# Performance work log

Measured on AMD Instinct MI355X. Metric: run time of the kernel, lower is better.

## Reference

```python
import jax, jax.numpy as jnp
import numpy as np

H, W = 512, 1024            # panorama resolution
GRID = 512                  # occupancy histogram resolution (height=width=512)
ABS_SCALE = 20000.0         # mm, ground-plane extent
UNIT_SCALE = 1000.0         # m -> mm
COUNT_TH = 100.0            # histogram count clamp


def _xyz_sphere(ref_plan):
    # Vectorized version of the original double loop.
    i = np.arange(H, dtype=np.float32)
    j = np.arange(W, dtype=np.float32)
    theta = -np.pi * (i / (H - 1) - 0.5)          # [H]
    phi = np.pi * (2.0 * j / (W - 1) - 1.0)       # [W]
    ct, st = np.cos(theta)[:, None], np.sin(theta)[:, None]   # [H,1]
    cp, sp = np.cos(phi)[None, :], np.sin(phi)[None, :]       # [1,W]
    if ref_plan == 'horizontal':
        P = np.stack([cp * ct, sp * ct, np.broadcast_to(st, (H, W))], 0)
    elif ref_plan == 'vertical':
        P = np.stack([cp * ct, np.broadcast_to(-st, (H, W)), sp * ct], 0)
    else:  # lateral
        P = np.stack([sp * ct, np.broadcast_to(-st, (H, W)), cp * ct], 0)
    return jnp.asarray(P.astype(np.float32))      # [3,H,W]

_SPHERES = [_xyz_sphere(p) for p in ('horizontal', 'vertical', 'lateral')]


def _density_one(depth_hw, sph):
    # depth_hw: [H,W]; sph: [3,H,W]
    ps = depth_hw[None] * sph                               # [3,H,W] 3D points
    xy = ps[:2].reshape(2, -1) * UNIT_SCALE                 # [2,N] mm, (x,y)
    coords = (xy + ABS_SCALE / 2.0) / ABS_SCALE * GRID      # [2,N] in grid units
    coords = jnp.clip(jnp.round(coords), 0.0, GRID - 1).astype(jnp.int32)
    flat = coords[1] * GRID + coords[0]                     # density[y, x]
    hist = jnp.zeros(GRID * GRID, jnp.float32).at[flat].add(1.0)
    hist = jnp.minimum(hist, COUNT_TH)
    hist = hist / jnp.max(hist)
    return hist.reshape(GRID, GRID)


def _density(depth, sph):
    # depth: [B,1,H,W] -> [B,GRID,GRID], batched scatter histogram
    return jax.vmap(_density_one, in_axes=(0, None))(depth[:, 0], sph)


def _inverse_huber(pred, gt):
    # berHu loss: L1 below c = 0.2*max|d|, scaled L2 above.
    diff = jnp.abs(pred - gt)
    c = 0.2 * jnp.max(diff)
    loss = jnp.where(diff <= c, diff, (diff * diff + c * c) / (2.0 * c))
    return jnp.mean(loss)


def setup_inputs() -> dict:
    key = jax.random.key(0)
    k1, k2 = jax.random.split(key)
    # indoor depths in [0, 10) meters so histogram bins are populated
    pred = jax.random.uniform(k1, (16, 1, H, W), jnp.float32) * 10.0
    gt = jax.random.uniform(k2, (16, 1, H, W), jnp.float32) * 10.0
    return {"pred_depth": pred, "gt_depth": gt}


def reference(pred_depth, gt_depth):
    total = jnp.float32(0.0)
    for sph in _SPHERES:  # fixed 3 projection planes
        pred_om = _density(pred_depth, sph)
        gt_om = _density(gt_depth, sph)
        total = total + _inverse_huber(pred_om, gt_om)
    return total
```

## Files before the change

kernel.cpp:

```cpp
#include <hip/hip_runtime.h>

#define PI_F 3.14159265358979323846f

#define MAXZ_OFF_B   24576
#define HIST_OFF_B   32768
#define BUCK_OFF_B   25198592
#define REGION_U16   12320

__device__ inline float div20000(float a) {
    const float r = 1.0f / 20000.0f;
    float q0 = a * r;
    float e = fmaf(-20000.0f, q0, a);
    return fmaf(e, r, q0);
}

__device__ inline int bin1(float v) {
    float f = rintf(div20000(v + 10000.0f) * 512.0f);
    return (int)fminf(fmaxf(f, 0.0f), 511.0f);
}

__global__ __launch_bounds__(256) void trig_kernel(
    float* __restrict__ tbl, unsigned* __restrict__ maxz,
    float* __restrict__ out) {
    const int t = threadIdx.x + blockIdx.x * 256;
    if (blockIdx.x == 0) {
        if (threadIdx.x < 128) maxz[threadIdx.x] = 0u;
        if (threadIdx.x == 128) out[0] = 0.0f;
    }
    if (t < 1024) {
        float fj = (float)t;
        float phi = PI_F * ((2.0f * fj) / 1023.0f - 1.0f);
        tbl[t] = cosf(phi);
        tbl[1024 + t] = sinf(phi);
    } else {
        int i = t - 1024;
        float fi = (float)i;
        float theta = -PI_F * (fi / 511.0f - 0.5f);
        tbl[2048 + i] = cosf(theta);
        tbl[2560 + i] = sinf(theta);
    }
}

__global__ __launch_bounds__(256) void bin_kernel(
    const float* __restrict__ pred, const float* __restrict__ gt,
    const float* __restrict__ tbl, unsigned short* __restrict__ buck) {
    __shared__ unsigned cnt[768];
    __shared__ unsigned bsum[24];
    __shared__ unsigned off[25];
    __shared__ __align__(16) unsigned short sdata[12288];
    const int tid = threadIdx.x, wg = blockIdx.x;
    const unsigned rep = (unsigned)(tid & 31);
    const int xcd = wg & 7, i4 = (wg >> 3) & 127, hh = wg >> 10;
    const int h = (hh << 3) | xcd;
    #pragma unroll
    for (int z = 0; z < 3; ++z) cnt[tid + (z << 8)] = 0u;
    const float4 cp4 = *(const float4*)&tbl[tid << 2];
    const float4 sp4 = *(const float4*)&tbl[1024 + (tid << 2)];
    const float4 ct4 = *(const float4*)&tbl[2048 + (i4 << 2)];
    const float4 st4 = *(const float4*)&tbl[2560 + (i4 << 2)];
    __syncthreads();
    const float* img = ((h >> 4) ? gt : pred) + ((h & 15) << 19);
    unsigned items[48];
    #pragma unroll
    for (int r = 0; r < 4; ++r) {
        const int i = i4 * 4 + r;
        const float4 d4 = *(const float4*)(img + (i << 10) + (tid << 2));
        const float ct = (&ct4.x)[r], st = (&st4.x)[r];
        #pragma unroll
        for (int k = 0; k < 4; ++k) {
            float d = (&d4.x)[k];
            float aA = (&cp4.x)[k] * ct;
            float aB = (&sp4.x)[k] * ct;
            float A = (d * aA) * 1000.0f;
            float B = (d * aB) * 1000.0f;
            float C = (d * (-st)) * 1000.0f;
            int iA = bin1(A), iB = bin1(B), iC = bin1(C);
            unsigned f0 = ((unsigned)iB << 9) | (unsigned)iA;
            unsigned f1 = ((unsigned)iC << 9) | (unsigned)iA;
            unsigned f2 = ((unsigned)iC << 9) | (unsigned)iB;
            unsigned b0 = f0 >> 15;
            unsigned b1 = 8u + (f1 >> 15);
            unsigned b2 = 16u + (f2 >> 15);
            unsigned r0 = atomicAdd(&cnt[(b0 << 5) | rep], 1u);
            unsigned r1 = atomicAdd(&cnt[(b1 << 5) | rep], 1u);
            unsigned r2 = atomicAdd(&cnt[(b2 << 5) | rep], 1u);
            const int base = (r * 4 + k) * 3;
            items[base + 0] = (b0 << 27) | (rep << 22) | (r0 << 15) | (f0 & 32767u);
            items[base + 1] = (b1 << 27) | (rep << 22) | (r1 << 15) | (f1 & 32767u);
            items[base + 2] = (b2 << 27) | (rep << 22) | (r2 << 15) | (f2 & 32767u);
        }
    }
    __syncthreads();
    if (tid < 24) {
        unsigned s = 0;
        #pragma unroll
        for (int r = 0; r < 32; ++r) {
            unsigned t = cnt[(tid << 5) | r];
            cnt[(tid << 5) | r] = s;
            s += t;
        }
        bsum[tid] = s;
    }
    __syncthreads();
    if (tid == 0) {
        unsigned s = 0;
        #pragma unroll
        for (int b = 0; b < 24; ++b) { off[b] = s; s += bsum[b]; }
        off[24] = s;
    }
    __syncthreads();
    if (tid < 24) {
        unsigned o = off[tid];
        #pragma unroll
        for (int r = 0; r < 32; ++r) cnt[(tid << 5) | r] += o;
    }
    __syncthreads();
    #pragma unroll
    for (int t = 0; t < 48; ++t) {
        const unsigned it = items[t];
        const unsigned slot = ((it >> 27) << 5) | ((it >> 22) & 31u);
        sdata[cnt[slot] + ((it >> 15) & 127u)] = (unsigned short)(it & 32767u);
    }
    __syncthreads();
    unsigned short* regG = buck + (size_t)wg * REGION_U16;
    if (tid < 25) regG[tid] = (unsigned short)off[tid];
    const uint4* s4p = (const uint4*)sdata;
    uint4* g4 = (uint4*)(regG + 32);
    #pragma unroll
    for (int c = 0; c < 6; ++c) g4[(c << 8) + tid] = s4p[(c << 8) + tid];
}

__global__ __launch_bounds__(1024, 8) void scan_kernel(
    const unsigned short* __restrict__ buck, unsigned* __restrict__ hp,
    unsigned* __restrict__ maxraw) {
    __shared__ unsigned lh[16384];
    __shared__ unsigned s4[16];
    const int tid = threadIdx.x, wg = blockIdx.x;
    const int xcd = wg & 7, hhi = (wg >> 3) & 3;
    const int X = wg >> 5;
    const int pair = X / 6, idx6 = X % 6;
    const int plane = idx6 >> 1;
    const int band = (idx6 & 1) ? (4 + pair) : (3 - pair);
    const int h = (hhi << 3) | xcd;
    const int bucket = plane * 8 + band;

    #pragma unroll
    for (int k = 0; k < 4; ++k)
        *(uint4*)&lh[(k << 12) + (tid << 2)] = make_uint4(0, 0, 0, 0);
    __syncthreads();

    const int wid = tid >> 6, lane = tid & 63;
    for (int i4 = wid; i4 < 128; i4 += 16) {
        const unsigned short* reg =
            buck + (size_t)(xcd | (i4 << 3) | (hhi << 10)) * REGION_U16;
        const int lo = reg[bucket], hi = reg[bucket + 1];
        const unsigned short* data = reg + 32;
        int a = (lo + 7) & ~7;
        if (a > hi) a = hi;
        const int head = a - lo;
        if (lane < head) {
            const unsigned id = data[lo + lane];
            atomicAdd(&lh[id >> 1], 1u << ((id & 1u) << 4));
        }
        const int nv = (hi - a) >> 3;
        for (int v = lane; v < nv; v += 64) {
            const uint4 w = *(const uint4*)&data[a + (v << 3)];
            unsigned prev = w.x & 65535u, c = 1;
            auto step = [&](unsigned id) {
                if (id == prev) { ++c; }
                else {
                    atomicAdd(&lh[prev >> 1], c << ((prev & 1u) << 4));
                    prev = id; c = 1;
                }
            };
            step(w.x >> 16);
            step(w.y & 65535u); step(w.y >> 16);
            step(w.z & 65535u); step(w.z >> 16);
            step(w.w & 65535u); step(w.w >> 16);
            atomicAdd(&lh[prev >> 1], c << ((prev & 1u) << 4));
        }
        const int tail = (hi - a) & 7;
        if (lane < tail) {
            const unsigned id = data[a + (nv << 3) + lane];
            atomicAdd(&lh[id >> 1], 1u << ((id & 1u) << 4));
        }
    }
    __syncthreads();

    unsigned m = 0;
    unsigned* gout = hp + ((plane * 32 + h) << 16) + (band << 13);
    #pragma unroll
    for (int k = 0; k < 8; ++k) {
        int w = (k << 10) + tid;
        unsigned v0 = lh[2 * w], v1 = lh[2 * w + 1];
        unsigned c0 = v0 & 65535u, c1 = v0 >> 16;
        unsigned c2 = v1 & 65535u, c3 = v1 >> 16;
        m = max(max(m, max(c0, c1)), max(c2, c3));
        gout[w] = min(c0, 255u) | (min(c1, 255u) << 8) |
                  (min(c2, 255u) << 16) | (min(c3, 255u) << 24);
    }
    #pragma unroll
    for (int o = 32; o; o >>= 1) m = max(m, (unsigned)__shfl_down((int)m, o));
    if ((tid & 63) == 0) s4[tid >> 6] = m;
    __syncthreads();
    if (tid == 0) {
        #pragma unroll
        for (int k = 1; k < 16; ++k) m = max(m, s4[k]);
        atomicMax(&maxraw[plane * 32 + h], m);
    }
}

__device__ inline float blockMaxF(float v) {
    #pragma unroll
    for (int o = 32; o; o >>= 1) v = fmaxf(v, __shfl_down(v, o));
    __shared__ float s[4];
    if ((threadIdx.x & 63) == 0) s[threadIdx.x >> 6] = v;
    __syncthreads();
    if (threadIdx.x == 0) v = fmaxf(fmaxf(s[0], s[1]), fmaxf(s[2], s[3]));
    return v;
}

__device__ inline float blockSumF(float v) {
    #pragma unroll
    for (int o = 32; o; o >>= 1) v += __shfl_down(v, o);
    __shared__ float s[4];
    if ((threadIdx.x & 63) == 0) s[threadIdx.x >> 6] = v;
    __syncthreads();
    if (threadIdx.x == 0) v = (s[0] + s[1]) + (s[2] + s[3]);
    return v;
}

__global__ void maxdiff_kernel(const unsigned* __restrict__ hp,
                               const unsigned* __restrict__ maxraw,
                               unsigned* __restrict__ maxdiff) {
    int blk = blockIdx.x;
    int b = blk & 15, chunk = (blk >> 4) & 15, plane = blk >> 8;
    const unsigned* P = hp + ((plane * 32 + b) << 16) + (chunk << 12);
    const unsigned* G = P + (16 << 16);
    float nP = fminf((float)maxraw[plane * 32 + b], 100.0f);
    float nG = fminf((float)maxraw[plane * 32 + 16 + b], 100.0f);
    float m = 0.0f;
    #pragma unroll
    for (int k = 0; k < 4; ++k) {
        uint4 wp = *(const uint4*)&P[(k << 10) + (threadIdx.x << 2)];
        uint4 wg = *(const uint4*)&G[(k << 10) + (threadIdx.x << 2)];
        #pragma unroll
        for (int w = 0; w < 4; ++w) {
            unsigned up = (&wp.x)[w], ug = (&wg.x)[w];
            #pragma unroll
            for (int s = 0; s < 32; s += 8) {
                float pn = fminf((float)((up >> s) & 255u), 100.0f) / nP;
                float gn = fminf((float)((ug >> s) & 255u), 100.0f) / nG;
                m = fmaxf(m, fabsf(pn - gn));
            }
        }
    }
    m = blockMaxF(m);
    if (threadIdx.x == 0) atomicMax(&maxdiff[plane], __float_as_uint(m));
}

__global__ void loss_kernel(const unsigned* __restrict__ hp,
                            const unsigned* __restrict__ maxraw,
                            const unsigned* __restrict__ maxdiff,
                            float* __restrict__ out) {
    int blk = blockIdx.x;
    int b = blk & 15, chunk = (blk >> 4) & 15, plane = blk >> 8;
    const unsigned* P = hp + ((plane * 32 + b) << 16) + (chunk << 12);
    const unsigned* G = P + (16 << 16);
    float c = 0.2f * __uint_as_float(maxdiff[plane]);
    float nP = fminf((float)maxraw[plane * 32 + b], 100.0f);
    float nG = fminf((float)maxraw[plane * 32 + 16 + b], 100.0f);
    float acc = 0.0f;
    #pragma unroll
    for (int k = 0; k < 4; ++k) {
        uint4 wp = *(const uint4*)&P[(k << 10) + (threadIdx.x << 2)];
        uint4 wg = *(const uint4*)&G[(k << 10) + (threadIdx.x << 2)];
        #pragma unroll
        for (int w = 0; w < 4; ++w) {
            unsigned up = (&wp.x)[w], ug = (&wg.x)[w];
            #pragma unroll
            for (int s = 0; s < 32; s += 8) {
                float pn = fminf((float)((up >> s) & 255u), 100.0f) / nP;
                float gn = fminf((float)((ug >> s) & 255u), 100.0f) / nG;
                float d = fabsf(pn - gn);
                acc += (d <= c) ? d : (d * d + c * c) / (2.0f * c);
            }
        }
    }
    acc = blockSumF(acc);
    if (threadIdx.x == 0) atomicAdd(out, acc / 4194304.0f);
}

extern "C" void kernel_launch(void* const* d_in, const int* in_sizes, int n_in,
                              void* d_out, int out_size, void* d_ws, size_t ws_size,
                              hipStream_t stream) {
    const float* pred = (const float*)d_in[0];
    const float* gt   = (const float*)d_in[1];
    float* out        = (float*)d_out;
    char* ws          = (char*)d_ws;

    float* tbl        = (float*)ws;
    unsigned* maxz    = (unsigned*)(ws + MAXZ_OFF_B);
    unsigned* maxraw  = maxz;
    unsigned* maxdiff = maxz + 96;
    unsigned* hp      = (unsigned*)(ws + HIST_OFF_B);
    unsigned short* buck = (unsigned short*)(ws + BUCK_OFF_B);

    trig_kernel<<<6, 256, 0, stream>>>(tbl, maxz, out);
    bin_kernel<<<4096, 256, 0, stream>>>(pred, gt, tbl, buck);
    scan_kernel<<<768, 1024, 0, stream>>>(buck, hp, maxraw);
    maxdiff_kernel<<<768, 256, 0, stream>>>(hp, maxraw, maxdiff);
    loss_kernel<<<768, 256, 0, stream>>>(hp, maxraw, maxdiff, out);
}
```

Baseline: 215.7 us.

## Split histogram into 16 row bands per plane with padded counters and prefetched offsets

The bin kernel now partitions each plane's 512x512 histogram into 16 bands of 32 rows instead of 8, and pads the per-bucket counter layout to stride 33 to avoid LDS bank conflicts. The scan kernel correspondingly uses half-size 32KB LDS histograms with 512 threads and twice as many blocks, aiming for higher occupancy. Each wave now walks 16 consecutive regions with software-prefetched bucket bounds instead of a strided loop. The trade-off is a larger per-region header and more bucket bookkeeping in the bin kernel.

```diff
diff --git a/kernel.cpp b/kernel.cpp
--- a/kernel.cpp
+++ b/kernel.cpp
@@ -5,7 +5,7 @@
 #define MAXZ_OFF_B   24576
 #define HIST_OFF_B   32768
 #define BUCK_OFF_B   25198592
-#define REGION_U16   12320
+#define REGION_U16   12336
 
 __device__ inline float div20000(float a) {
     const float r = 1.0f / 20000.0f;
@@ -44,16 +44,19 @@
 __global__ __launch_bounds__(256) void bin_kernel(
     const float* __restrict__ pred, const float* __restrict__ gt,
     const float* __restrict__ tbl, unsigned short* __restrict__ buck) {
-    __shared__ unsigned cnt[768];
-    __shared__ unsigned bsum[24];
-    __shared__ unsigned off[25];
+    __shared__ unsigned cnt[1584];
+    __shared__ unsigned bsum[48];
+    __shared__ unsigned off[49];
     __shared__ __align__(16) unsigned short sdata[12288];
     const int tid = threadIdx.x, wg = blockIdx.x;
     const unsigned rep = (unsigned)(tid & 31);
     const int xcd = wg & 7, i4 = (wg >> 3) & 127, hh = wg >> 10;
     const int h = (hh << 3) | xcd;
     #pragma unroll
-    for (int z = 0; z < 3; ++z) cnt[tid + (z << 8)] = 0u;
+    for (int z = 0; z < 7; ++z) {
+        int idx = tid + (z << 8);
+        if (idx < 1584) cnt[idx] = 0u;
+    }
     const float4 cp4 = *(const float4*)&tbl[tid << 2];
     const float4 sp4 = *(const float4*)&tbl[1024 + (tid << 2)];
     const float4 ct4 = *(const float4*)&tbl[2048 + (i4 << 2)];
@@ -78,25 +81,25 @@
             unsigned f0 = ((unsigned)iB << 9) | (unsigned)iA;
             unsigned f1 = ((unsigned)iC << 9) | (unsigned)iA;
             unsigned f2 = ((unsigned)iC << 9) | (unsigned)iB;
-            unsigned b0 = f0 >> 15;
-            unsigned b1 = 8u + (f1 >> 15);
-            unsigned b2 = 16u + (f2 >> 15);
-            unsigned r0 = atomicAdd(&cnt[(b0 << 5) | rep], 1u);
-            unsigned r1 = atomicAdd(&cnt[(b1 << 5) | rep], 1u);
-            unsigned r2 = atomicAdd(&cnt[(b2 << 5) | rep], 1u);
+            unsigned b0 = f0 >> 14;
+            unsigned b1 = 16u + (f1 >> 14);
+            unsigned b2 = 32u + (f2 >> 14);
+            unsigned r0 = atomicAdd(&cnt[b0 * 33u + rep], 1u);
+            unsigned r1 = atomicAdd(&cnt[b1 * 33u + rep], 1u);
+            unsigned r2 = atomicAdd(&cnt[b2 * 33u + rep], 1u);
             const int base = (r * 4 + k) * 3;
-            items[base + 0] = (b0 << 27) | (rep << 22) | (r0 << 15) | (f0 & 32767u);
-            items[base + 1] = (b1 << 27) | (rep << 22) | (r1 << 15) | (f1 & 32767u);
-            items[base + 2] = (b2 << 27) | (rep << 22) | (r2 << 15) | (f2 & 32767u);
-        }
-    }
-    __syncthreads();
-    if (tid < 24) {
+            items[base + 0] = (b0 << 26) | (rep << 21) | (r0 << 14) | (f0 & 16383u);
+            items[base + 1] = (b1 << 26) | (rep << 21) | (r1 << 14) | (f1 & 16383u);
+            items[base + 2] = (b2 << 26) | (rep << 21) | (r2 << 14) | (f2 & 16383u);
+        }
+    }
+    __syncthreads();
+    if (tid < 48) {
         unsigned s = 0;
         #pragma unroll
         for (int r = 0; r < 32; ++r) {
-            unsigned t = cnt[(tid << 5) | r];
-            cnt[(tid << 5) | r] = s;
+            unsigned t = cnt[tid * 33 + r];
+            cnt[tid * 33 + r] = s;
             s += t;
         }
         bsum[tid] = s;
@@ -105,56 +108,63 @@
     if (tid == 0) {
         unsigned s = 0;
         #pragma unroll
-        for (int b = 0; b < 24; ++b) { off[b] = s; s += bsum[b]; }
-        off[24] = s;
-    }
-    __syncthreads();
-    if (tid < 24) {
+        for (int b = 0; b < 48; ++b) { off[b] = s; s += bsum[b]; }
+        off[48] = s;
+    }
+    __syncthreads();
+    if (tid < 48) {
         unsigned o = off[tid];
         #pragma unroll
-        for (int r = 0; r < 32; ++r) cnt[(tid << 5) | r] += o;
+        for (int r = 0; r < 32; ++r) cnt[tid * 33 + r] += o;
     }
     __syncthreads();
     #pragma unroll
     for (int t = 0; t < 48; ++t) {
         const unsigned it = items[t];
-        const unsigned slot = ((it >> 27) << 5) | ((it >> 22) & 31u);
-        sdata[cnt[slot] + ((it >> 15) & 127u)] = (unsigned short)(it & 32767u);
+        const unsigned slot = (it >> 26) * 33u + ((it >> 21) & 31u);
+        sdata[cnt[slot] + ((it >> 14) & 127u)] = (unsigned short)(it & 16383u);
     }
     __syncthreads();
     unsigned short* regG = buck + (size_t)wg * REGION_U16;
-    if (tid < 25) regG[tid] = (unsigned short)off[tid];
+    if (tid < 48) regG[tid] = (unsigned short)off[tid + 1];
     const uint4* s4p = (const uint4*)sdata;
-    uint4* g4 = (uint4*)(regG + 32);
+    uint4* g4 = (uint4*)(regG + 48);
     #pragma unroll
     for (int c = 0; c < 6; ++c) g4[(c << 8) + tid] = s4p[(c << 8) + tid];
 }
 
-__global__ __launch_bounds__(1024, 8) void scan_kernel(
+__global__ __launch_bounds__(512, 8) void scan_kernel(
     const unsigned short* __restrict__ buck, unsigned* __restrict__ hp,
     unsigned* __restrict__ maxraw) {
-    __shared__ unsigned lh[16384];
-    __shared__ unsigned s4[16];
+    __shared__ unsigned lh[8192];
+    __shared__ unsigned s4[8];
     const int tid = threadIdx.x, wg = blockIdx.x;
     const int xcd = wg & 7, hhi = (wg >> 3) & 3;
     const int X = wg >> 5;
-    const int pair = X / 6, idx6 = X % 6;
-    const int plane = idx6 >> 1;
-    const int band = (idx6 & 1) ? (4 + pair) : (3 - pair);
+    const int plane = X % 3;
+    const unsigned long long PACKED = 0xF0E1D2C3B4A59687ULL;
+    const int band = (int)((PACKED >> ((X / 3) * 4)) & 15);
     const int h = (hhi << 3) | xcd;
-    const int bucket = plane * 8 + band;
+    const int bucket = plane * 16 + band;
 
     #pragma unroll
     for (int k = 0; k < 4; ++k)
-        *(uint4*)&lh[(k << 12) + (tid << 2)] = make_uint4(0, 0, 0, 0);
+        *(uint4*)&lh[(k << 11) + (tid << 2)] = make_uint4(0, 0, 0, 0);
     __syncthreads();
 
     const int wid = tid >> 6, lane = tid & 63;
-    for (int i4 = wid; i4 < 128; i4 += 16) {
-        const unsigned short* reg =
-            buck + (size_t)(xcd | (i4 << 3) | (hhi << 10)) * REGION_U16;
-        const int lo = reg[bucket], hi = reg[bucket + 1];
-        const unsigned short* data = reg + 32;
+    const unsigned short* reg =
+        buck + (size_t)(xcd | ((wid << 4) << 3) | (hhi << 10)) * REGION_U16;
+    int lo = bucket ? reg[bucket - 1] : 0;
+    int hi = reg[bucket];
+    for (int jj = 0; jj < 16; ++jj) {
+        const unsigned short* data = reg + 48;
+        const unsigned short* nreg = reg + 8 * (size_t)REGION_U16;
+        int nlo = 0, nhi = 0;
+        if (jj < 15) {
+            nlo = bucket ? nreg[bucket - 1] : 0;
+            nhi = nreg[bucket];
+        }
         int a = (lo + 7) & ~7;
         if (a > hi) a = hi;
         const int head = a - lo;
@@ -184,14 +194,15 @@
             const unsigned id = data[a + (nv << 3) + lane];
             atomicAdd(&lh[id >> 1], 1u << ((id & 1u) << 4));
         }
+        reg = nreg; lo = nlo; hi = nhi;
     }
     __syncthreads();
 
     unsigned m = 0;
-    unsigned* gout = hp + ((plane * 32 + h) << 16) + (band << 13);
+    unsigned* gout = hp + ((plane * 32 + h) << 16) + (band << 12);
     #pragma unroll
     for (int k = 0; k < 8; ++k) {
-        int w = (k << 10) + tid;
+        int w = (k << 9) + tid;
         unsigned v0 = lh[2 * w], v1 = lh[2 * w + 1];
         unsigned c0 = v0 & 65535u, c1 = v0 >> 16;
         unsigned c2 = v1 & 65535u, c3 = v1 >> 16;
@@ -205,7 +216,7 @@
     __syncthreads();
     if (tid == 0) {
         #pragma unroll
-        for (int k = 1; k < 16; ++k) m = max(m, s4[k]);
+        for (int k = 1; k < 8; ++k) m = max(m, s4[k]);
         atomicMax(&maxraw[plane * 32 + h], m);
     }
 }
@@ -308,7 +319,7 @@
 
     trig_kernel<<<6, 256, 0, stream>>>(tbl, maxz, out);
     bin_kernel<<<4096, 256, 0, stream>>>(pred, gt, tbl, buck);
-    scan_kernel<<<768, 1024, 0, stream>>>(buck, hp, maxraw);
+    scan_kernel<<<1536, 512, 0, stream>>>(buck, hp, maxraw);
     maxdiff_kernel<<<768, 256, 0, stream>>>(hp, maxraw, maxdiff);
     loss_kernel<<<768, 256, 0, stream>>>(hp, maxraw, maxdiff, out);
 }
```

After: 254.0 us. +17.8%, slower.
